# Kernel optimization log

Hardware: AMD Instinct MI355X
Metric: run time of the kernel (lower is better)

Reference implementation:

```python
import jax, jax.numpy as jnp
import numpy as np

N_OSC = 256
BATCH = 1024
DT = 0.1
STEPS = 10


def setup_inputs() -> dict:
    key = jax.random.key(0)
    k_theta, k_K, k_omega = jax.random.split(key, 3)
    theta_init = jax.random.normal(k_theta, (BATCH, N_OSC), dtype=jnp.float32)
    K0 = jax.random.normal(k_K, (N_OSC, N_OSC), dtype=jnp.float32) * 0.1
    K = (K0 + K0.T) / 2  # symmetric coupling matrix, as in torch init
    omega = jax.random.normal(k_omega, (N_OSC,), dtype=jnp.float32) * 0.1
    K_global = jnp.float32(0.5)
    return {"theta_init": theta_init, "K": K, "omega": omega, "K_global": K_global}


def reference(theta_init, K, omega, K_global):
    n = K.shape[0]

    def step(theta, _):
        # diff[b, i, j] = theta[b, j] - theta[b, i]
        diff = theta[..., None, :] - theta[..., :, None]
        coupling_sum = jnp.sum(K * jnp.sin(diff), axis=-1)  # (batch, n)
        dtheta = omega + (K_global / n) * coupling_sum
        theta_new = theta + DT * dtheta
        # wrap to (-pi, pi]
        theta_new = jnp.arctan2(jnp.sin(theta_new), jnp.cos(theta_new))
        return theta_new, None

    theta, _ = jax.lax.scan(step, theta_init, None, length=STEPS)
    cos_mean = jnp.cos(theta).mean(axis=-1)
    sin_mean = jnp.sin(theta).mean(axis=-1)
    coherence = jnp.sqrt(cos_mean ** 2 + sin_mean ** 2)
    return theta, coherence
```

## Files before the change

kernel.cpp:

```cpp
#include <hip/hip_runtime.h>
#include <math.h>


typedef __attribute__((ext_vector_type(4))) float f32x4;

constexpr int N       = 256;
constexpr int RB      = 16;
constexpr int STEPS   = 10;
constexpr int WAVES   = 8;
constexpr int THREADS = WAVES * 64;
constexpr float DT    = 0.1f;
constexpr float TWO_PI     = 6.28318530717958648f;
constexpr float INV_TWO_PI = 0.15915494309189535f;

__global__ __launch_bounds__(THREADS, 2)
void kuramoto_fp8(const float* __restrict__ theta0,
                  const float* __restrict__ Kmat,
                  const float* __restrict__ omega,
                  const float* __restrict__ kglob,
                  float* __restrict__ theta_out,
                  float* __restrict__ coh_out)
{
    __shared__ __align__(16) unsigned char SC[2][RB][512];
    __shared__ float redS[RB][WAVES], redC[RB][WAVES];

    const int tid  = threadIdx.x;
    const int wv   = tid >> 6;
    const int lane = tid & 63;
    const int q    = lane >> 4;
    const int l15  = lane & 15;
    const int b0   = blockIdx.x * RB;

    const float kgn = kglob[0] * (1.0f / 256.0f);

    long kf[2][8];
#pragma unroll
    for (int t = 0; t < 2; ++t) {
        const int i = 32 * wv + 16 * t + l15;
        const float* kr = Kmat + (size_t)i * N + 8 * q;
#pragma unroll
        for (int c = 0; c < 8; ++c) {
            float4 lo = *(const float4*)(kr + 32 * c);
            float4 hi = *(const float4*)(kr + 32 * c + 4);
            int w0 = __builtin_amdgcn_cvt_pk_fp8_f32(lo.x, lo.y, 0, false);
            w0     = __builtin_amdgcn_cvt_pk_fp8_f32(lo.z, lo.w, w0, true);
            int w1 = __builtin_amdgcn_cvt_pk_fp8_f32(hi.x, hi.y, 0, false);
            w1     = __builtin_amdgcn_cvt_pk_fp8_f32(hi.z, hi.w, w1, true);
            kf[t][c] = (long)(unsigned)w0 | ((long)w1 << 32);
        }
    }

    float thv[2][4], om[2][4];
#pragma unroll
    for (int t = 0; t < 2; ++t)
#pragma unroll
        for (int r = 0; r < 4; ++r) {
            const int i = 32 * wv + 16 * t + 4 * q + r;
            om[t][r]  = omega[i];
            thv[t][r] = theta0[(size_t)(b0 + l15) * N + i];
        }

    float sv[2][4], cv[2][4];

    for (int s = 0; s < STEPS; ++s) {
        const int buf = s & 1;
#pragma unroll
        for (int t = 0; t < 2; ++t) {
#pragma unroll
            for (int r = 0; r < 4; ++r)
                __sincosf(thv[t][r], &sv[t][r], &cv[t][r]);
            int spk = __builtin_amdgcn_cvt_pk_fp8_f32(sv[t][0], sv[t][1], 0, false);
            spk     = __builtin_amdgcn_cvt_pk_fp8_f32(sv[t][2], sv[t][3], spk, true);
            int cpk = __builtin_amdgcn_cvt_pk_fp8_f32(cv[t][0], cv[t][1], 0, false);
            cpk     = __builtin_amdgcn_cvt_pk_fp8_f32(cv[t][2], cv[t][3], cpk, true);
            const int g = 8 * wv + 4 * t + q;
            const int u = (g >> 1) ^ l15;
            int2 val; val.x = spk; val.y = cpk;
            *(int2*)&SC[buf][l15][16 * u + 8 * (g & 1)] = val;
        }
        __syncthreads();

        f32x4 aS[2], aC[2];
#pragma unroll
        for (int t = 0; t < 2; ++t) {
            aS[t] = (f32x4){0.f, 0.f, 0.f, 0.f};
            aC[t] = (f32x4){0.f, 0.f, 0.f, 0.f};
        }
#pragma unroll
        for (int c = 0; c < 8; ++c) {
            const int uu = (4 * c + q) ^ l15;
            int4 vvv = *(const int4*)&SC[buf][l15][16 * uu];
            long Bs = (long)(unsigned)vvv.x | ((long)vvv.z << 32);
            long Bc = (long)(unsigned)vvv.y | ((long)vvv.w << 32);
#pragma unroll
            for (int t = 0; t < 2; ++t) {
                aS[t] = __builtin_amdgcn_mfma_f32_16x16x32_fp8_fp8(kf[t][c], Bs, aS[t], 0, 0, 0);
                aC[t] = __builtin_amdgcn_mfma_f32_16x16x32_fp8_fp8(kf[t][c], Bc, aC[t], 0, 0, 0);
            }
        }

#pragma unroll
        for (int t = 0; t < 2; ++t)
#pragma unroll
            for (int r = 0; r < 4; ++r) {
                float coup = cv[t][r] * aS[t][r] - sv[t][r] * aC[t][r];
                thv[t][r] = fmaf(DT, fmaf(kgn, coup, om[t][r]), thv[t][r]);
            }
    }

    float ps = 0.f, pc = 0.f;
#pragma unroll
    for (int t = 0; t < 2; ++t)
#pragma unroll
        for (int r = 0; r < 4; ++r) {
            float th = thv[t][r];
            float s0, c0;
            __sincosf(th, &s0, &c0);
            float w = fmaf(-TWO_PI, rintf(th * INV_TWO_PI), th);
            theta_out[(size_t)(b0 + l15) * N + 32 * wv + 16 * t + 4 * q + r] = w;
            ps += s0; pc += c0;
        }
    ps += __shfl_xor(ps, 16, 64);  pc += __shfl_xor(pc, 16, 64);
    ps += __shfl_xor(ps, 32, 64);  pc += __shfl_xor(pc, 32, 64);
    if (q == 0) { redS[l15][wv] = ps; redC[l15][wv] = pc; }
    __syncthreads();
    if (tid < RB) {
        float S = 0.f, C = 0.f;
#pragma unroll
        for (int k = 0; k < WAVES; ++k) { S += redS[tid][k]; C += redC[tid][k]; }
        float sm = S * (1.0f / 256.0f);
        float cm = C * (1.0f / 256.0f);
        coh_out[b0 + tid] = sqrtf(sm * sm + cm * cm);
    }
}

extern "C" void kernel_launch(void* const* d_in, const int* in_sizes, int n_in,
                              void* d_out, int out_size, void* d_ws, size_t ws_size,
                              hipStream_t stream) {
    const float* theta0 = (const float*)d_in[0];
    const float* Kmat   = (const float*)d_in[1];
    const float* omega  = (const float*)d_in[2];
    const float* kglob  = (const float*)d_in[3];

    float* theta_out = (float*)d_out;
    float* coh_out   = theta_out + 1024 * N;

    kuramoto_fp8<<<dim3(1024 / RB), dim3(THREADS), 0, stream>>>(
        theta0, Kmat, omega, kglob, theta_out, coh_out);
}
```

Baseline: 75.19 us.

## Replace per-step sincos with Taylor rotation update and double waves per block

Instead of evaluating sincos of theta every step, the kernel carries sin/cos and advances them with a small-angle rotation built from a truncated Taylor series of the step increment. Waves per block go from 8 to 16, so each wave owns 16 oscillators and issues half the MFMAs, split across two accumulators to shorten the dependency chain. Theta loads and stores become float4 vector accesses. The Taylor rotation adds approximation error that can accumulate over the steps, and the final sin/cos used for coherence come from the rotated values rather than a fresh evaluation.

```diff
diff --git a/kernel.cpp b/kernel.cpp
--- a/kernel.cpp
+++ b/kernel.cpp
@@ -7,14 +7,14 @@
 constexpr int N       = 256;
 constexpr int RB      = 16;
 constexpr int STEPS   = 10;
-constexpr int WAVES   = 8;
+constexpr int WAVES   = 16;
 constexpr int THREADS = WAVES * 64;
 constexpr float DT    = 0.1f;
 constexpr float TWO_PI     = 6.28318530717958648f;
 constexpr float INV_TWO_PI = 0.15915494309189535f;
 
-__global__ __launch_bounds__(THREADS, 2)
-void kuramoto_fp8(const float* __restrict__ theta0,
+__global__ __launch_bounds__(THREADS, 4)
+void kuramoto_rot(const float* __restrict__ theta0,
                   const float* __restrict__ Kmat,
                   const float* __restrict__ omega,
                   const float* __restrict__ kglob,
@@ -33,11 +33,9 @@
 
     const float kgn = kglob[0] * (1.0f / 256.0f);
 
-    long kf[2][8];
-#pragma unroll
-    for (int t = 0; t < 2; ++t) {
-        const int i = 32 * wv + 16 * t + l15;
-        const float* kr = Kmat + (size_t)i * N + 8 * q;
+    long kf[8];
+    {
+        const float* kr = Kmat + (size_t)(16 * wv + l15) * N + 8 * q;
 #pragma unroll
         for (int c = 0; c < 8; ++c) {
             float4 lo = *(const float4*)(kr + 32 * c);
@@ -46,80 +44,71 @@
             w0     = __builtin_amdgcn_cvt_pk_fp8_f32(lo.z, lo.w, w0, true);
             int w1 = __builtin_amdgcn_cvt_pk_fp8_f32(hi.x, hi.y, 0, false);
             w1     = __builtin_amdgcn_cvt_pk_fp8_f32(hi.z, hi.w, w1, true);
-            kf[t][c] = (long)(unsigned)w0 | ((long)w1 << 32);
+            kf[c] = (long)(unsigned)w0 | ((long)w1 << 32);
         }
     }
 
-    float thv[2][4], om[2][4];
+    const int oscB = 16 * wv + 4 * q;
+    float4 th4 = *(const float4*)(theta0 + (size_t)(b0 + l15) * N + oscB);
+    float4 om4 = *(const float4*)(omega + oscB);
+    float th[4] = {th4.x, th4.y, th4.z, th4.w};
+    float om[4] = {om4.x, om4.y, om4.z, om4.w};
+    float sn[4], cs[4];
 #pragma unroll
-    for (int t = 0; t < 2; ++t)
-#pragma unroll
-        for (int r = 0; r < 4; ++r) {
-            const int i = 32 * wv + 16 * t + 4 * q + r;
-            om[t][r]  = omega[i];
-            thv[t][r] = theta0[(size_t)(b0 + l15) * N + i];
-        }
+    for (int r = 0; r < 4; ++r)
+        __sincosf(th[r], &sn[r], &cs[r]);
 
-    float sv[2][4], cv[2][4];
+    const int g     = 4 * wv + q;
+    const int wrOff = 16 * ((g >> 1) ^ l15) + 8 * (g & 1);
 
     for (int s = 0; s < STEPS; ++s) {
         const int buf = s & 1;
-#pragma unroll
-        for (int t = 0; t < 2; ++t) {
-#pragma unroll
-            for (int r = 0; r < 4; ++r)
-                __sincosf(thv[t][r], &sv[t][r], &cv[t][r]);
-            int spk = __builtin_amdgcn_cvt_pk_fp8_f32(sv[t][0], sv[t][1], 0, false);
-            spk     = __builtin_amdgcn_cvt_pk_fp8_f32(sv[t][2], sv[t][3], spk, true);
-            int cpk = __builtin_amdgcn_cvt_pk_fp8_f32(cv[t][0], cv[t][1], 0, false);
-            cpk     = __builtin_amdgcn_cvt_pk_fp8_f32(cv[t][2], cv[t][3], cpk, true);
-            const int g = 8 * wv + 4 * t + q;
-            const int u = (g >> 1) ^ l15;
-            int2 val; val.x = spk; val.y = cpk;
-            *(int2*)&SC[buf][l15][16 * u + 8 * (g & 1)] = val;
-        }
+        int spk = __builtin_amdgcn_cvt_pk_fp8_f32(sn[0], sn[1], 0, false);
+        spk     = __builtin_amdgcn_cvt_pk_fp8_f32(sn[2], sn[3], spk, true);
+        int cpk = __builtin_amdgcn_cvt_pk_fp8_f32(cs[0], cs[1], 0, false);
+        cpk     = __builtin_amdgcn_cvt_pk_fp8_f32(cs[2], cs[3], cpk, true);
+        int2 val; val.x = spk; val.y = cpk;
+        *(int2*)&SC[buf][l15][wrOff] = val;
         __syncthreads();
 
         f32x4 aS[2], aC[2];
-#pragma unroll
-        for (int t = 0; t < 2; ++t) {
-            aS[t] = (f32x4){0.f, 0.f, 0.f, 0.f};
-            aC[t] = (f32x4){0.f, 0.f, 0.f, 0.f};
-        }
+        aS[0] = (f32x4){0.f,0.f,0.f,0.f}; aS[1] = (f32x4){0.f,0.f,0.f,0.f};
+        aC[0] = (f32x4){0.f,0.f,0.f,0.f}; aC[1] = (f32x4){0.f,0.f,0.f,0.f};
 #pragma unroll
         for (int c = 0; c < 8; ++c) {
-            const int uu = (4 * c + q) ^ l15;
-            int4 vvv = *(const int4*)&SC[buf][l15][16 * uu];
-            long Bs = (long)(unsigned)vvv.x | ((long)vvv.z << 32);
-            long Bc = (long)(unsigned)vvv.y | ((long)vvv.w << 32);
-#pragma unroll
-            for (int t = 0; t < 2; ++t) {
-                aS[t] = __builtin_amdgcn_mfma_f32_16x16x32_fp8_fp8(kf[t][c], Bs, aS[t], 0, 0, 0);
-                aC[t] = __builtin_amdgcn_mfma_f32_16x16x32_fp8_fp8(kf[t][c], Bc, aC[t], 0, 0, 0);
-            }
+            int4 v = *(const int4*)&SC[buf][l15][16 * (((4 * c + q) ^ l15))];
+            long Bs = (long)(unsigned)v.x | ((long)v.z << 32);
+            long Bc = (long)(unsigned)v.y | ((long)v.w << 32);
+            aS[c & 1] = __builtin_amdgcn_mfma_f32_16x16x32_fp8_fp8(kf[c], Bs, aS[c & 1], 0, 0, 0);
+            aC[c & 1] = __builtin_amdgcn_mfma_f32_16x16x32_fp8_fp8(kf[c], Bc, aC[c & 1], 0, 0, 0);
         }
 
 #pragma unroll
-        for (int t = 0; t < 2; ++t)
-#pragma unroll
-            for (int r = 0; r < 4; ++r) {
-                float coup = cv[t][r] * aS[t][r] - sv[t][r] * aC[t][r];
-                thv[t][r] = fmaf(DT, fmaf(kgn, coup, om[t][r]), thv[t][r]);
-            }
+        for (int r = 0; r < 4; ++r) {
+            float gS = aS[0][r] + aS[1][r];
+            float gC = aC[0][r] + aC[1][r];
+            float coup = cs[r] * gS - sn[r] * gC;
+            float d  = DT * fmaf(kgn, coup, om[r]);
+            float d2 = d * d;
+            float sd = d * fmaf(d2, -1.0f / 6.0f, 1.0f);
+            float cd = fmaf(d2, fmaf(d2, 1.0f / 24.0f, -0.5f), 1.0f);
+            float s2 = fmaf(sn[r], cd,  cs[r] * sd);
+            float c2 = fmaf(cs[r], cd, -sn[r] * sd);
+            sn[r] = s2; cs[r] = c2; th[r] += d;
+        }
     }
 
     float ps = 0.f, pc = 0.f;
+    float4 outv;
+    float wr[4];
 #pragma unroll
-    for (int t = 0; t < 2; ++t)
-#pragma unroll
-        for (int r = 0; r < 4; ++r) {
-            float th = thv[t][r];
-            float s0, c0;
-            __sincosf(th, &s0, &c0);
-            float w = fmaf(-TWO_PI, rintf(th * INV_TWO_PI), th);
-            theta_out[(size_t)(b0 + l15) * N + 32 * wv + 16 * t + 4 * q + r] = w;
-            ps += s0; pc += c0;
-        }
+    for (int r = 0; r < 4; ++r) {
+        wr[r] = fmaf(-TWO_PI, rintf(th[r] * INV_TWO_PI), th[r]);
+        ps += sn[r]; pc += cs[r];
+    }
+    outv.x = wr[0]; outv.y = wr[1]; outv.z = wr[2]; outv.w = wr[3];
+    *(float4*)(theta_out + (size_t)(b0 + l15) * N + oscB) = outv;
+
     ps += __shfl_xor(ps, 16, 64);  pc += __shfl_xor(pc, 16, 64);
     ps += __shfl_xor(ps, 32, 64);  pc += __shfl_xor(pc, 32, 64);
     if (q == 0) { redS[l15][wv] = ps; redC[l15][wv] = pc; }
@@ -145,6 +134,6 @@
     float* theta_out = (float*)d_out;
     float* coh_out   = theta_out + 1024 * N;
 
-    kuramoto_fp8<<<dim3(1024 / RB), dim3(THREADS), 0, stream>>>(
+    kuramoto_rot<<<dim3(1024 / RB), dim3(THREADS), 0, stream>>>(
         theta0, Kmat, omega, kglob, theta_out, coh_out);
 }
```

New measurement: 77.00 us. 2.4% more time.
